# Optimization experiments

Measured on AMD Instinct MI355X. Metric: run time of the kernel, lower is better.

## Reference

```python
import math
import jax, jax.numpy as jnp
import numpy as np

V = 50257; T = 1024; D = 1024; H = 16; L = 4; DS = 3; B = 2
DH = D // H; DF = 4 * D
PEN = 1.0; EW = 0.01; FW = 0.1; RW = 0.01


def setup_inputs() -> dict:
    key = jax.random.key(0)
    ks = jax.random.split(key, 12)
    p = lambda k, s: jax.random.normal(k, s, jnp.float32) * 0.02
    return dict(
        idx=jax.random.randint(ks[0], (B, T), 0, V),
        targets=jax.random.randint(ks[1], (B, T), 0, V),
        emb=p(ks[2], (V, D)),                      # tied token emb / lm_head
        pos_emb=p(ks[3], (T, D)),
        positions=jax.random.normal(ks[4], (L, T, DS)) * 0.3,
        ln1_g=jnp.ones((L, D)), ln1_b=jnp.zeros((L, D)),
        ln2_g=jnp.ones((L, D)), ln2_b=jnp.zeros((L, D)),
        lnf_g=jnp.ones((D,)), lnf_b=jnp.zeros((D,)),
        qkv_w=p(ks[5], (L, D, 3 * D)),             # stored [in,out] (= torch W.T)
        proj_w=p(ks[6], (L, D, D)),
        w1=p(ks[7], (L, D, DF)), b1=jnp.zeros((L, DF)),
        w2=p(ks[8], (L, DF, D)), b2=jnp.zeros((L, D)),
    )


def _ln(x, g, b, eps=1e-5):
    m = x.mean(-1, keepdims=True)
    v = ((x - m) ** 2).mean(-1, keepdims=True)
    return (x - m) * jax.lax.rsqrt(v + eps) * g + b


def _safe_dists(pos):
    # pairwise L2 distance with zero (not nan) gradient on the diagonal
    diff = pos[:, None, :] - pos[None, :, :]      # [T,T,DS]
    sq = (diff ** 2).sum(-1)
    return jnp.where(sq > 0, jnp.sqrt(jnp.where(sq > 0, sq, 1.0)), 0.0)


def reference(idx, targets, emb, pos_emb, positions, ln1_g, ln1_b, ln2_g, ln2_b,
              lnf_g, lnf_b, qkv_w, proj_w, w1, b1, w2, b2):
    x = emb[idx] + pos_emb[None, :, :]            # [B,T,D]; dropout = identity (eval)
    causal = jnp.triu(jnp.ones((T, T), bool), 1)
    offd = ~jnp.eye(T, dtype=bool)
    scale = 1.0 / math.sqrt(DH)
    tde = jnp.float32(0.0); tfe = jnp.float32(0.0); tre = jnp.float32(0.0)
    all_w = []; all_d = []
    for l in range(L):
        h = _ln(x, ln1_g[l], ln1_b[l])
        q, k, v = jnp.split(h @ qkv_w[l], 3, axis=-1)
        rs = lambda t: t.reshape(B, T, H, DH).transpose(0, 2, 1, 3)  # [B,H,T,DH]
        q, k, v = rs(q), rs(k), rs(v)
        logits_a = jnp.einsum('bhid,bhjd->bhij', q, k) * scale
        dists = _safe_dists(positions[l])                       # [T,T]
        logits_a = logits_a - PEN * dists
        logits_a = jnp.where(causal, -jnp.inf, logits_a)
        w = jax.nn.softmax(logits_a, axis=-1)                   # [B,H,T,T]
        tde = tde + (w * dists).sum(-1).mean()
        tfe = tfe + (-(w * jnp.log(w + 1e-9)).sum(-1)).mean()
        tre = tre + jnp.where(offd, 1.0 / (dists + 1e-4), 0.0).sum() / (T * T - T)
        out = jnp.einsum('bhij,bhjd->bhid', w, v).transpose(0, 2, 1, 3).reshape(B, T, D)
        x = x + out @ proj_w[l]
        h2 = _ln(x, ln2_g[l], ln2_b[l])
        x = x + (jax.nn.gelu(h2 @ w1[l] + b1[l], approximate=False) @ w2[l] + b2[l])
        all_w.append(jax.lax.stop_gradient(w))
        all_d.append(jax.lax.stop_gradient(dists))
    logits = _ln(x, lnf_g, lnf_b) @ emb.T                       # tied lm_head
    logp = jax.nn.log_softmax(logits, axis=-1)
    ce = -jnp.take_along_axis(logp, targets[..., None], axis=-1).mean()
    loss = ce + EW * tde + FW * tfe + RW * tre
    return (logits, loss, tde, tfe, tre, tuple(all_w), tuple(all_d))
```

## Files before the change

kernel.cpp:

```cpp
#include <hip/hip_runtime.h>
#include <hip/hip_bf16.h>
#include <cmath>

#define TT 1024
#define DD 1024
#define HH 16
#define LL 4
#define BB 2
#define DHH 64
#define DFF 4096
#define VV 50257

typedef float floatx4 __attribute__((ext_vector_type(4)));
typedef __bf16 bf16x8 __attribute__((ext_vector_type(8)));

typedef unsigned int u32;
typedef __attribute__((address_space(1))) const u32 gu32;
typedef __attribute__((address_space(3))) u32 lu32;

__device__ __forceinline__ void gload16(const unsigned short* g, unsigned short* l) {
  __builtin_amdgcn_global_load_lds((gu32*)g, (lu32*)l, 16, 0, 0);
}

__device__ __forceinline__ unsigned short f2bf(float f) {
  unsigned u = __float_as_uint(f);
  u += 0x7fffu + ((u >> 16) & 1u);
  return (unsigned short)(u >> 16);
}
__device__ __forceinline__ float bf2f(unsigned short u) {
  return __uint_as_float(((unsigned)u) << 16);
}

__device__ __forceinline__ float wave_sum(float v) {
#pragma unroll
  for (int off = 1; off < 64; off <<= 1) v += __shfl_xor(v, off);
  return v;
}
__device__ __forceinline__ float wave_max(float v) {
#pragma unroll
  for (int off = 1; off < 64; off <<= 1) v = fmaxf(v, __shfl_xor(v, off));
  return v;
}

#define EPI_F32 0
#define EPI_QKV 1
#define EPI_ATT 2
#define EPI_GELU 3
#define EPI_LSE 4
#define EPI_SBF 5

struct GemmArgs {
  const unsigned short* A;
  const unsigned short* B;
  long aBatch, bBatch, cBatch;
  int M, N, K, ldc;
  float* outF;
  unsigned short* q;
  unsigned short* kk;
  unsigned short* vt;
  unsigned short* outB;
  const float* bias;
  float2* lsePart;
  int pn;
  int kchunk;
};

template <int EPI>
__global__ __launch_bounds__(256) void gemm_kernel(GemmArgs ga) {
  __shared__ __align__(16) unsigned short As[128 * 32];
  __shared__ __align__(16) unsigned short Bs[128 * 32];
  const int tid = threadIdx.x;
  int bm, bn;
  if constexpr (EPI == EPI_SBF) {
    const int xb = blockIdx.x;
    int r = (int)((sqrtf(8.f * xb + 1.f) - 1.f) * 0.5f);
    if ((r * (r + 1)) / 2 > xb) --r;
    else if (((r + 1) * (r + 2)) / 2 <= xb) ++r;
    const int c = xb - (r * (r + 1)) / 2;
    bm = r * 128; bn = c * 128;
  } else {
    bm = blockIdx.y * 128; bn = blockIdx.x * 128;
  }
  const int z = blockIdx.z;
  const unsigned short* A = ga.A + (long)z * ga.aBatch;
  const unsigned short* Bp = ga.B + (long)z * ga.bBatch;
  const int K = ga.K, N = ga.N;

  int kbeg = 0, kend = K;
  if (ga.kchunk) { kbeg = z * ga.kchunk; kend = kbeg + ga.kchunk; }

  floatx4 acc[4][4];
#pragma unroll
  for (int i = 0; i < 4; ++i)
#pragma unroll
    for (int j = 0; j < 4; ++j) acc[i][j] = (floatx4){0.f, 0.f, 0.f, 0.f};

  const int lane = tid & 63, wave = tid >> 6;
  const int wm = (wave & 1) * 64, wn = (wave >> 1) * 64;
  const int fr = lane & 15, quad = lane >> 4;
  const int srow = tid >> 2;
  const int sc8 = (tid & 3) * 8;

  unsigned short* lA0 = &As[wave * 512];
  unsigned short* lA1 = &As[2048 + wave * 512];
  unsigned short* lB0 = &Bs[wave * 512];
  unsigned short* lB1 = &Bs[2048 + wave * 512];

  for (int k0 = kbeg; k0 < kend; k0 += 32) {
    const long ra = (long)(bm + srow) * K + (k0 + sc8);
    const long rb = (long)(bn + srow) * K + (k0 + sc8);
    gload16(A + ra, lA0);
    gload16(A + ra + 64L * K, lA1);
    gload16(Bp + rb, lB0);
    gload16(Bp + rb + 64L * K, lB1);
    __syncthreads();
    bf16x8 af[4], bfr[4];
#pragma unroll
    for (int i = 0; i < 4; ++i) af[i] = *(const bf16x8*)(&As[(wm + i * 16 + fr) * 32 + quad * 8]);
#pragma unroll
    for (int j = 0; j < 4; ++j) bfr[j] = *(const bf16x8*)(&Bs[(wn + j * 16 + fr) * 32 + quad * 8]);
#pragma unroll
    for (int i = 0; i < 4; ++i)
#pragma unroll
      for (int j = 0; j < 4; ++j)
        acc[i][j] = __builtin_amdgcn_mfma_f32_16x16x32_bf16(af[i], bfr[j], acc[i][j], 0, 0, 0);
    __syncthreads();
  }

  if constexpr (EPI == EPI_LSE) {
    float2* sm = (float2*)As;
#pragma unroll
    for (int i = 0; i < 4; ++i) {
#pragma unroll
      for (int r = 0; r < 4; ++r) {
        const int m = bm + wm + i * 16 + quad * 4 + r;
        float mx = -INFINITY, ss = 0.f;
#pragma unroll
        for (int j = 0; j < 4; ++j) {
          const int n = bn + wn + j * 16 + fr;
          const float val = acc[i][j][r];
          float v;
          if (n < N) { ga.outF[(long)m * ga.ldc + n] = val; v = val; }
          else v = -INFINITY;
          if (v > mx) { ss = ss * __expf(mx - v) + 1.f; mx = v; }
          else ss += __expf(v - mx);
        }
#pragma unroll
        for (int off = 1; off < 16; off <<= 1) {
          const float mo = __shfl_xor(mx, off), so = __shfl_xor(ss, off);
          const float M = fmaxf(mx, mo);
          ss = ss * __expf(mx - M) + so * __expf(mo - M);
          mx = M;
        }
        if (fr == 0) {
          const int rl = wm + i * 16 + quad * 4 + r;
          sm[rl * 2 + (wave >> 1)] = make_float2(mx, ss);
        }
      }
    }
    __syncthreads();
    if (tid < 128) {
      const float2 a = sm[tid * 2], b = sm[tid * 2 + 1];
      const float M = fmaxf(a.x, b.x);
      const float S = a.y * __expf(a.x - M) + b.y * __expf(b.x - M);
      ga.lsePart[(long)(bm + tid) * ga.pn + blockIdx.x] = make_float2(M, S);
    }
  } else {
#pragma unroll
    for (int i = 0; i < 4; ++i) {
#pragma unroll
      for (int j = 0; j < 4; ++j) {
        const int n = bn + wn + j * 16 + fr;
#pragma unroll
        for (int r = 0; r < 4; ++r) {
          const int m = bm + wm + i * 16 + quad * 4 + r;
          const float val = acc[i][j][r];
          if constexpr (EPI == EPI_F32) {
            if (n < N) ga.outF[(long)z * ga.cBatch + (long)m * ga.ldc + n] = val;
          }
          if constexpr (EPI == EPI_SBF) {
            ga.outB[(long)z * TT * TT + (long)m * TT + n] = f2bf(val);
          }
          if constexpr (EPI == EPI_QKV) {
            const int b = m >> 10, t = m & 1023;
            const int sec = n >> 10, col = n & 1023;
            const int hd = col >> 6, dh = col & 63;
            const unsigned short bv = f2bf(val);
            if (sec == 0)      ga.q [((long)(b * HH + hd) * TT + t) * DHH + dh] = bv;
            else if (sec == 1) ga.kk[((long)(b * HH + hd) * TT + t) * DHH + dh] = bv;
            else               ga.vt[((long)(b * HH + hd) * DHH + dh) * TT + t] = bv;
          }
          if constexpr (EPI == EPI_ATT) {
            if (n < 64) {
              const int b = z >> 4, hd = z & 15;
              ga.outB[((long)(b * TT + m)) * DD + hd * DHH + n] = f2bf(val);
            }
          }
          if constexpr (EPI == EPI_GELU) {
            const float xx = val + ga.bias[n];
            const float gl = 0.5f * xx * (1.f + erff(xx * 0.7071067811865475f));
            ga.outB[(long)m * DFF + n] = f2bf(gl);
          }
        }
      }
    }
  }
}

__global__ __launch_bounds__(256) void transpose_bf16_kernel(const float* __restrict__ src,
    unsigned short* __restrict__ dst, int R, int C) {
  __shared__ float tile[32][33];
  const int c0 = blockIdx.x * 32, r0 = blockIdx.y * 32;
  const int tx = threadIdx.x & 31, ty = threadIdx.x >> 5;
#pragma unroll
  for (int rr = ty; rr < 32; rr += 8)
    tile[rr][tx] = src[(long)(r0 + rr) * C + (c0 + tx)];
  __syncthreads();
#pragma unroll
  for (int rr = ty; rr < 32; rr += 8)
    dst[(long)(c0 + rr) * R + (r0 + tx)] = f2bf(tile[tx][rr]);
}

__global__ __launch_bounds__(256) void convert_bf16_kernel(const float* __restrict__ in,
    unsigned short* __restrict__ out) {
  const long i = (long)blockIdx.x * 256 + threadIdx.x;
  const float4 v = ((const float4*)in)[i];
  ushort4 o;
  o.x = f2bf(v.x); o.y = f2bf(v.y); o.z = f2bf(v.z); o.w = f2bf(v.w);
  ((ushort4*)out)[i] = o;
}

__global__ __launch_bounds__(256) void embed_kernel(const int* __restrict__ idx,
    const float* __restrict__ emb, const float* __restrict__ pos, float* __restrict__ x) {
  const int bt = blockIdx.x;
  const int t = bt & (TT - 1);
  const int tok = idx[bt];
  const float4 e = ((const float4*)(emb + (long)tok * DD))[threadIdx.x];
  const float4 p = ((const float4*)(pos + (long)t * DD))[threadIdx.x];
  float4 o; o.x = e.x + p.x; o.y = e.y + p.y; o.z = e.z + p.z; o.w = e.w + p.w;
  ((float4*)(x + (long)bt * DD))[threadIdx.x] = o;
}

__global__ __launch_bounds__(256) void ln_kernel(const float* __restrict__ x,
    const float* __restrict__ g, const float* __restrict__ b, unsigned short* __restrict__ out) {
  const int row = blockIdx.x;
  const float4 v = ((const float4*)(x + (long)row * DD))[threadIdx.x];
  float s = v.x + v.y + v.z + v.w;
  float s2 = v.x * v.x + v.y * v.y + v.z * v.z + v.w * v.w;
  s = wave_sum(s); s2 = wave_sum(s2);
  __shared__ float ps[4], ps2[4];
  const int wv = threadIdx.x >> 6, lane = threadIdx.x & 63;
  if (lane == 0) { ps[wv] = s; ps2[wv] = s2; }
  __syncthreads();
  s = ps[0] + ps[1] + ps[2] + ps[3];
  s2 = ps2[0] + ps2[1] + ps2[2] + ps2[3];
  const float mean = s * (1.f / DD);
  const float var = s2 * (1.f / DD) - mean * mean;
  const float rs = rsqrtf(var + 1e-5f);
  const float4 gv = ((const float4*)g)[threadIdx.x];
  const float4 bv = ((const float4*)b)[threadIdx.x];
  ushort4 o;
  o.x = f2bf((v.x - mean) * rs * gv.x + bv.x);
  o.y = f2bf((v.y - mean) * rs * gv.y + bv.y);
  o.z = f2bf((v.z - mean) * rs * gv.z + bv.z);
  o.w = f2bf((v.w - mean) * rs * gv.w + bv.w);
  ((ushort4*)(out + (long)row * DD))[threadIdx.x] = o;
}

__global__ __launch_bounds__(256) void ln_fuse_kernel(float* __restrict__ x,
    const float* __restrict__ p0, const float* __restrict__ p1,
    const float* __restrict__ bias,
    const float* __restrict__ g, const float* __restrict__ b,
    unsigned short* __restrict__ out) {
  const int row = blockIdx.x;
  float4 v = ((const float4*)(x + (long)row * DD))[threadIdx.x];
  const float4 a0 = ((const float4*)(p0 + (long)row * DD))[threadIdx.x];
  const float4 a1 = ((const float4*)(p1 + (long)row * DD))[threadIdx.x];
  v.x += a0.x + a1.x; v.y += a0.y + a1.y; v.z += a0.z + a1.z; v.w += a0.w + a1.w;
  if (bias) {
    const float4 bb = ((const float4*)bias)[threadIdx.x];
    v.x += bb.x; v.y += bb.y; v.z += bb.z; v.w += bb.w;
  }
  ((float4*)(x + (long)row * DD))[threadIdx.x] = v;
  float s = v.x + v.y + v.z + v.w;
  float s2 = v.x * v.x + v.y * v.y + v.z * v.z + v.w * v.w;
  s = wave_sum(s); s2 = wave_sum(s2);
  __shared__ float ps[4], ps2[4];
  const int wv = threadIdx.x >> 6, lane = threadIdx.x & 63;
  if (lane == 0) { ps[wv] = s; ps2[wv] = s2; }
  __syncthreads();
  s = ps[0] + ps[1] + ps[2] + ps[3];
  s2 = ps2[0] + ps2[1] + ps2[2] + ps2[3];
  const float mean = s * (1.f / DD);
  const float var = s2 * (1.f / DD) - mean * mean;
  const float rs = rsqrtf(var + 1e-5f);
  const float4 gv = ((const float4*)g)[threadIdx.x];
  const float4 bv = ((const float4*)b)[threadIdx.x];
  ushort4 o;
  o.x = f2bf((v.x - mean) * rs * gv.x + bv.x);
  o.y = f2bf((v.y - mean) * rs * gv.y + bv.y);
  o.z = f2bf((v.z - mean) * rs * gv.z + bv.z);
  o.w = f2bf((v.w - mean) * rs * gv.w + bv.w);
  ((ushort4*)(out + (long)row * DD))[threadIdx.x] = o;
}

__global__ __launch_bounds__(256) void dists_kernel(const float* __restrict__ pos,
    float* __restrict__ dout, float* __restrict__ tre_acc) {
  const int i = blockIdx.x;
  const float px = pos[i * 3], py = pos[i * 3 + 1], pz = pos[i * 3 + 2];
  float rsum = 0.f;
#pragma unroll
  for (int c = 0; c < 4; ++c) {
    const int j = c * 256 + threadIdx.x;
    const float dx = px - pos[j * 3];
    const float dy = py - pos[j * 3 + 1];
    const float dz = pz - pos[j * 3 + 2];
    const float sq = dx * dx + dy * dy + dz * dz;
    const float d = sq > 0.f ? sqrtf(sq) : 0.f;
    dout[(long)i * TT + j] = d;
    if (j != i) rsum += 1.f / (d + 1e-4f);
  }
  rsum = wave_sum(rsum);
  __shared__ float ps[4];
  const int wv = threadIdx.x >> 6, lane = threadIdx.x & 63;
  if (lane == 0) ps[wv] = rsum;
  __syncthreads();
  if (threadIdx.x == 0) atomicAdd(tre_acc, ps[0] + ps[1] + ps[2] + ps[3]);
}

__global__ __launch_bounds__(256) void softmax_kernel(unsigned short* __restrict__ wb,
    const float* __restrict__ dists, float* __restrict__ W,
    float2* __restrict__ partials) {
  const long row = blockIdx.x;
  const int i = (int)(row & (TT - 1));
  unsigned short* sr = wb + row * TT;
  const float* dr = dists + (long)i * TT;
  const int j0 = threadIdx.x * 4;

  const float4 dv = ((const float4*)dr)[threadIdx.x];
  const ushort4 su = ((const ushort4*)sr)[threadIdx.x];
  float d[4] = {dv.x, dv.y, dv.z, dv.w};
  float sa[4] = {bf2f(su.x), bf2f(su.y), bf2f(su.z), bf2f(su.w)};
  float l[4];
  float mx = -INFINITY;
#pragma unroll
  for (int c = 0; c < 4; ++c) {
    float v = sa[c] * 0.125f - d[c];
    if (j0 + c > i) v = -INFINITY;
    l[c] = v;
    mx = fmaxf(mx, v);
  }
  mx = wave_max(mx);
  __shared__ float rmax[4], rsm[4], rwd[4], rent[4];
  const int wv = threadIdx.x >> 6, lane = threadIdx.x & 63;
  if (lane == 0) rmax[wv] = mx;
  __syncthreads();
  mx = fmaxf(fmaxf(rmax[0], rmax[1]), fmaxf(rmax[2], rmax[3]));
  float e[4], sum = 0.f;
#pragma unroll
  for (int c = 0; c < 4; ++c) { e[c] = __expf(l[c] - mx); sum += e[c]; }
  sum = wave_sum(sum);
  if (lane == 0) rsm[wv] = sum;
  __syncthreads();
  sum = rsm[0] + rsm[1] + rsm[2] + rsm[3];
  const float inv = 1.f / sum;
  float4 wo;
  ushort4 bo;
  const float w0 = e[0] * inv, w1 = e[1] * inv, w2 = e[2] * inv, w3 = e[3] * inv;
  wo.x = w0; wo.y = w1; wo.z = w2; wo.w = w3;
  bo.x = f2bf(w0); bo.y = f2bf(w1); bo.z = f2bf(w2); bo.w = f2bf(w3);
  float wd = w0 * d[0] + w1 * d[1] + w2 * d[2] + w3 * d[3];
  float ent = -(w0 * __logf(w0 + 1e-9f) + w1 * __logf(w1 + 1e-9f)
        + w2 * __logf(w2 + 1e-9f) + w3 * __logf(w3 + 1e-9f));
  ((float4*)(W + row * TT))[threadIdx.x] = wo;
  ((ushort4*)sr)[threadIdx.x] = bo;
  wd = wave_sum(wd); ent = wave_sum(ent);
  if (lane == 0) { rwd[wv] = wd; rent[wv] = ent; }
  __syncthreads();
  if (threadIdx.x == 0) {
    partials[row] = make_float2(rwd[0] + rwd[1] + rwd[2] + rwd[3],
                                rent[0] + rent[1] + rent[2] + rent[3]);
  }
}

__global__ __launch_bounds__(256) void reduce_partials_kernel(const float2* __restrict__ p,
    int n, float* __restrict__ tde_acc, float* __restrict__ tfe_acc) {
  float wd = 0.f, ent = 0.f;
  for (int i = blockIdx.x * 256 + threadIdx.x; i < n; i += gridDim.x * 256) {
    const float2 v = p[i];
    wd += v.x; ent += v.y;
  }
  wd = wave_sum(wd); ent = wave_sum(ent);
  __shared__ float pw[4], pe[4];
  const int wv = threadIdx.x >> 6, lane = threadIdx.x & 63;
  if (lane == 0) { pw[wv] = wd; pe[wv] = ent; }
  __syncthreads();
  if (threadIdx.x == 0) {
    atomicAdd(tde_acc, pw[0] + pw[1] + pw[2] + pw[3]);
    atomicAdd(tfe_acc, pe[0] + pe[1] + pe[2] + pe[3]);
  }
}

__global__ __launch_bounds__(256) void ce_reduce_kernel(const float2* __restrict__ part,
    const float* __restrict__ logits, const int* __restrict__ targets,
    float* __restrict__ ce_acc, int pn) {
  const int row = blockIdx.x;
  const float2* pr = part + (long)row * pn;
  float m = -INFINITY, s = 0.f;
  for (int i = threadIdx.x; i < pn; i += 256) {
    const float2 v = pr[i];
    const float M = fmaxf(m, v.x);
    s = s * __expf(m - M) + v.y * __expf(v.x - M);
    m = M;
  }
#pragma unroll
  for (int off = 1; off < 64; off <<= 1) {
    const float mo = __shfl_xor(m, off), so = __shfl_xor(s, off);
    const float M = fmaxf(m, mo);
    s = s * __expf(m - M) + so * __expf(mo - M);
    m = M;
  }
  __shared__ float pm[4], psv[4];
  const int wv = threadIdx.x >> 6, lane = threadIdx.x & 63;
  if (lane == 0) { pm[wv] = m; psv[wv] = s; }
  __syncthreads();
  if (threadIdx.x == 0) {
    const float M = fmaxf(fmaxf(pm[0], pm[1]), fmaxf(pm[2], pm[3]));
    const float S = psv[0] * __expf(pm[0] - M) + psv[1] * __expf(pm[1] - M)
                  + psv[2] * __expf(pm[2] - M) + psv[3] * __expf(pm[3] - M);
    atomicAdd(ce_acc, M + logf(S) - logits[(long)row * VV + targets[row]]);
  }
}

__global__ void zero_acc_kernel(float* p) { if (threadIdx.x < 4) p[threadIdx.x] = 0.f; }

__global__ void finalize_kernel(const float* __restrict__ acc, float* __restrict__ o) {
  if (threadIdx.x == 0) {
    const float tde = acc[0] * (1.f / 32768.f);
    const float tfe = acc[1] * (1.f / 32768.f);
    const float tre = acc[2] * (1.f / 1047552.f);
    const float ce = acc[3] * (1.f / 2048.f);
    o[0] = ce + 0.01f * tde + 0.1f * tfe + 0.01f * tre;
    o[1] = tde; o[2] = tfe; o[3] = tre;
  }
}

extern "C" void kernel_launch(void* const* d_in, const int* in_sizes, int n_in,
                              void* d_out, int out_size, void* d_ws, size_t ws_size,
                              hipStream_t stream) {
  const int* idx = (const int*)d_in[0];
  const int* targets = (const int*)d_in[1];
  const float* emb = (const float*)d_in[2];
  const float* pos_emb = (const float*)d_in[3];
  const float* positions = (const float*)d_in[4];
  const float* ln1_g = (const float*)d_in[5];
  const float* ln1_b = (const float*)d_in[6];
  const float* ln2_g = (const float*)d_in[7];
  const float* ln2_b = (const float*)d_in[8];
  const float* lnf_g = (const float*)d_in[9];
  const float* lnf_b = (const float*)d_in[10];
  const float* qkv_w = (const float*)d_in[11];
  const float* proj_w = (const float*)d_in[12];
  const float* w1 = (const float*)d_in[13];
  const float* b1 = (const float*)d_in[14];
  const float* w2 = (const float*)d_in[15];
  const float* b2 = (const float*)d_in[16];

  float* out = (float*)d_out;
  char* ws = (char*)d_ws;

  const long LOGITS_N = (long)BB * TT * VV;
  const long SCAL_OFF = LOGITS_N;
  const long ALLW_OFF = LOGITS_N + 4;
  const long ALLW_STRIDE = (long)BB * HH * TT * TT;
  const long ALLD_OFF = ALLW_OFF + 4 * ALLW_STRIDE;
  const long ALLD_STRIDE = (long)TT * TT;

  unsigned short* wt_qkv  = (unsigned short*)(ws);
  unsigned short* wt_proj = (unsigned short*)(ws + 25165824L);
  unsigned short* wt_w1   = (unsigned short*)(ws + 33554432L);
  unsigned short* wt_w2   = (unsigned short*)(ws + 67108864L);
  unsigned short* emb_bf  = (unsigned short*)(ws + 100663296L);
  float*          x       = (float*)(ws + 203589632L);
  unsigned short* h_bf    = (unsigned short*)(ws + 211978240L);
  unsigned short* q_bf    = (unsigned short*)(ws + 216172544L);
  unsigned short* k_bf    = (unsigned short*)(ws + 220366848L);
  unsigned short* vt_bf   = (unsigned short*)(ws + 224561152L);
  unsigned short* attb_bf = (unsigned short*)(ws + 228755456L);
  unsigned short* g_bf    = (unsigned short*)(ws + 232949760L);
  unsigned short* w_bf    = (unsigned short*)(ws + 249726976L);
  float*          accs    = (float*)(ws + 316835840L);

  float2* smpart = (float2*)attb_bf;
  float2* lsepart = (float2*)wt_qkv;
  float* pp = (float*)w_bf;
  float* fp = (float*)w_bf + 2L * 2048 * DD;
  const long RES_PART = (long)2048 * DD;
  const int LSE_PN = (VV + 127) / 128;

  const dim3 blk(256);

  for (int l = 0; l < LL; ++l) {
    transpose_bf16_kernel<<<dim3(3 * DD / 32, DD / 32), blk, 0, stream>>>(
        qkv_w + (long)l * DD * 3 * DD, wt_qkv + (long)l * 3 * DD * DD, DD, 3 * DD);
    transpose_bf16_kernel<<<dim3(DD / 32, DD / 32), blk, 0, stream>>>(
        proj_w + (long)l * DD * DD, wt_proj + (long)l * DD * DD, DD, DD);
    transpose_bf16_kernel<<<dim3(DFF / 32, DD / 32), blk, 0, stream>>>(
        w1 + (long)l * DD * DFF, wt_w1 + (long)l * DFF * DD, DD, DFF);
    transpose_bf16_kernel<<<dim3(DD / 32, DFF / 32), blk, 0, stream>>>(
        w2 + (long)l * DFF * DD, wt_w2 + (long)l * DD * DFF, DFF, DD);
  }
  convert_bf16_kernel<<<VV, blk, 0, stream>>>(emb, emb_bf);

  embed_kernel<<<BB * TT, blk, 0, stream>>>(idx, emb, pos_emb, x);
  zero_acc_kernel<<<1, 64, 0, stream>>>(accs);

  for (int l = 0; l < LL; ++l) {
    float* allw_l = out + ALLW_OFF + (long)l * ALLW_STRIDE;
    float* alld_l = out + ALLD_OFF + (long)l * ALLD_STRIDE;

    dists_kernel<<<TT, blk, 0, stream>>>(positions + (long)l * TT * 3, alld_l, accs + 2);
    if (l == 0)
      ln_kernel<<<BB * TT, blk, 0, stream>>>(x, ln1_g, ln1_b, h_bf);
    else
      ln_fuse_kernel<<<BB * TT, blk, 0, stream>>>(x, fp, fp + RES_PART,
          b2 + (long)(l - 1) * DD, ln1_g + l * DD, ln1_b + l * DD, h_bf);

    { GemmArgs ga = {}; ga.A = h_bf; ga.B = wt_qkv + (long)l * 3 * DD * DD;
      ga.M = BB * TT; ga.N = 3 * DD; ga.K = DD;
      ga.q = q_bf; ga.kk = k_bf; ga.vt = vt_bf;
      gemm_kernel<EPI_QKV><<<dim3(24, 16, 1), blk, 0, stream>>>(ga); }

    { GemmArgs ga = {}; ga.A = q_bf; ga.B = k_bf;
      ga.aBatch = (long)TT * DHH; ga.bBatch = (long)TT * DHH;
      ga.M = TT; ga.N = TT; ga.K = DHH;
      ga.outB = w_bf;
      gemm_kernel<EPI_SBF><<<dim3(36, 1, BB * HH), blk, 0, stream>>>(ga); }

    softmax_kernel<<<BB * HH * TT, blk, 0, stream>>>(w_bf, alld_l, allw_l, smpart);
    reduce_partials_kernel<<<64, blk, 0, stream>>>(smpart, BB * HH * TT, accs + 0, accs + 1);

    { GemmArgs ga = {}; ga.A = w_bf; ga.B = vt_bf;
      ga.aBatch = (long)TT * TT; ga.bBatch = (long)DHH * TT;
      ga.M = TT; ga.N = DHH; ga.K = TT;
      ga.outB = attb_bf;
      gemm_kernel<EPI_ATT><<<dim3(1, 8, BB * HH), blk, 0, stream>>>(ga); }

    { GemmArgs ga = {}; ga.A = attb_bf; ga.B = wt_proj + (long)l * DD * DD;
      ga.M = BB * TT; ga.N = DD; ga.K = DD; ga.ldc = DD;
      ga.outF = pp; ga.cBatch = RES_PART; ga.kchunk = DD / 2;
      gemm_kernel<EPI_F32><<<dim3(8, 16, 2), blk, 0, stream>>>(ga); }

    ln_fuse_kernel<<<BB * TT, blk, 0, stream>>>(x, pp, pp + RES_PART,
        nullptr, ln2_g + l * DD, ln2_b + l * DD, h_bf);

    { GemmArgs ga = {}; ga.A = h_bf; ga.B = wt_w1 + (long)l * DFF * DD;
      ga.M = BB * TT; ga.N = DFF; ga.K = DD;
      ga.bias = b1 + (long)l * DFF; ga.outB = g_bf;
      gemm_kernel<EPI_GELU><<<dim3(32, 16, 1), blk, 0, stream>>>(ga); }

    { GemmArgs ga = {}; ga.A = g_bf; ga.B = wt_w2 + (long)l * DD * DFF;
      ga.M = BB * TT; ga.N = DD; ga.K = DFF; ga.ldc = DD;
      ga.outF = fp; ga.cBatch = RES_PART; ga.kchunk = DFF / 2;
      gemm_kernel<EPI_F32><<<dim3(8, 16, 2), blk, 0, stream>>>(ga); }
  }

  ln_fuse_kernel<<<BB * TT, blk, 0, stream>>>(x, fp, fp + RES_PART,
      b2 + (long)(LL - 1) * DD, lnf_g, lnf_b, h_bf);

  { GemmArgs ga = {}; ga.A = h_bf; ga.B = emb_bf;
    ga.M = BB * TT; ga.N = VV; ga.K = DD;
    ga.outF = out; ga.ldc = VV; ga.cBatch = 0;
    ga.lsePart = lsepart; ga.pn = LSE_PN;
    gemm_kernel<EPI_LSE><<<dim3(LSE_PN, 16, 1), blk, 0, stream>>>(ga); }

  ce_reduce_kernel<<<BB * TT, blk, 0, stream>>>(lsepart, out, targets, accs + 3, LSE_PN);
  finalize_kernel<<<1, 64, 0, stream>>>(accs, out + SCAL_OFF);
}
```

Before: 2.741 ms.

## Skip masked K range in attention GEMM, stream outputs, batch weight transposes

In the attention-times-V GEMM, the K loop now stops at the end of the row block, because causal weights past the diagonal are zero. The LSE epilogue of the logits GEMM becomes a two-pass max-then-sum, and large fp32 outputs (logits and softmax weights) use nontemporal stores to avoid polluting the cache. The sixteen per-layer weight transpose launches become four batched launches using gridDim.z. The K truncation assumes the zero-padded structure of the weights buffer holds exactly, and any kchunk split interacting with it could produce wrong sums.

```diff
diff --git a/kernel.cpp b/kernel.cpp
--- a/kernel.cpp
+++ b/kernel.cpp
@@ -88,6 +88,9 @@
 
   int kbeg = 0, kend = K;
   if (ga.kchunk) { kbeg = z * ga.kchunk; kend = kbeg + ga.kchunk; }
+  if constexpr (EPI == EPI_ATT) {
+    kend = bm + 128;
+  }
 
   floatx4 acc[4][4];
 #pragma unroll
@@ -134,24 +137,26 @@
 #pragma unroll
       for (int r = 0; r < 4; ++r) {
         const int m = bm + wm + i * 16 + quad * 4 + r;
-        float mx = -INFINITY, ss = 0.f;
+        float mx = -INFINITY;
 #pragma unroll
         for (int j = 0; j < 4; ++j) {
           const int n = bn + wn + j * 16 + fr;
-          const float val = acc[i][j][r];
-          float v;
-          if (n < N) { ga.outF[(long)m * ga.ldc + n] = val; v = val; }
-          else v = -INFINITY;
-          if (v > mx) { ss = ss * __expf(mx - v) + 1.f; mx = v; }
-          else ss += __expf(v - mx);
+          if (n < N) {
+            const float val = acc[i][j][r];
+            __builtin_nontemporal_store(val, &ga.outF[(long)m * ga.ldc + n]);
+            mx = fmaxf(mx, val);
+          }
         }
 #pragma unroll
-        for (int off = 1; off < 16; off <<= 1) {
-          const float mo = __shfl_xor(mx, off), so = __shfl_xor(ss, off);
-          const float M = fmaxf(mx, mo);
-          ss = ss * __expf(mx - M) + so * __expf(mo - M);
-          mx = M;
+        for (int off = 1; off < 16; off <<= 1) mx = fmaxf(mx, __shfl_xor(mx, off));
+        float ss = 0.f;
+#pragma unroll
+        for (int j = 0; j < 4; ++j) {
+          const int n = bn + wn + j * 16 + fr;
+          if (n < N) ss += __expf(acc[i][j][r] - mx);
         }
+#pragma unroll
+        for (int off = 1; off < 16; off <<= 1) ss += __shfl_xor(ss, off);
         if (fr == 0) {
           const int rl = wm + i * 16 + quad * 4 + r;
           sm[rl * 2 + (wave >> 1)] = make_float2(mx, ss);
@@ -207,8 +212,10 @@
   }
 }
 
-__global__ __launch_bounds__(256) void transpose_bf16_kernel(const float* __restrict__ src,
-    unsigned short* __restrict__ dst, int R, int C) {
+__global__ __launch_bounds__(256) void transpose_bf16_kernel(const float* __restrict__ src0,
+    unsigned short* __restrict__ dst0, int R, int C, long sStride, long dStride) {
+  const float* src = src0 + (long)blockIdx.z * sStride;
+  unsigned short* dst = dst0 + (long)blockIdx.z * dStride;
   __shared__ float tile[32][33];
   const int c0 = blockIdx.x * 32, r0 = blockIdx.y * 32;
   const int tx = threadIdx.x & 31, ty = threadIdx.x >> 5;
@@ -364,15 +371,15 @@
   __syncthreads();
   sum = rsm[0] + rsm[1] + rsm[2] + rsm[3];
   const float inv = 1.f / sum;
-  float4 wo;
+  floatx4 wo;
   ushort4 bo;
   const float w0 = e[0] * inv, w1 = e[1] * inv, w2 = e[2] * inv, w3 = e[3] * inv;
-  wo.x = w0; wo.y = w1; wo.z = w2; wo.w = w3;
+  wo[0] = w0; wo[1] = w1; wo[2] = w2; wo[3] = w3;
   bo.x = f2bf(w0); bo.y = f2bf(w1); bo.z = f2bf(w2); bo.w = f2bf(w3);
   float wd = w0 * d[0] + w1 * d[1] + w2 * d[2] + w3 * d[3];
   float ent = -(w0 * __logf(w0 + 1e-9f) + w1 * __logf(w1 + 1e-9f)
         + w2 * __logf(w2 + 1e-9f) + w3 * __logf(w3 + 1e-9f));
-  ((float4*)(W + row * TT))[threadIdx.x] = wo;
+  __builtin_nontemporal_store(wo, (floatx4*)(W + row * TT) + threadIdx.x);
   ((ushort4*)sr)[threadIdx.x] = bo;
   wd = wave_sum(wd); ent = wave_sum(ent);
   if (lane == 0) { rwd[wv] = wd; rent[wv] = ent; }
@@ -500,16 +507,14 @@
 
   const dim3 blk(256);
 
-  for (int l = 0; l < LL; ++l) {
-    transpose_bf16_kernel<<<dim3(3 * DD / 32, DD / 32), blk, 0, stream>>>(
-        qkv_w + (long)l * DD * 3 * DD, wt_qkv + (long)l * 3 * DD * DD, DD, 3 * DD);
-    transpose_bf16_kernel<<<dim3(DD / 32, DD / 32), blk, 0, stream>>>(
-        proj_w + (long)l * DD * DD, wt_proj + (long)l * DD * DD, DD, DD);
-    transpose_bf16_kernel<<<dim3(DFF / 32, DD / 32), blk, 0, stream>>>(
-        w1 + (long)l * DD * DFF, wt_w1 + (long)l * DFF * DD, DD, DFF);
-    transpose_bf16_kernel<<<dim3(DD / 32, DFF / 32), blk, 0, stream>>>(
-        w2 + (long)l * DFF * DD, wt_w2 + (long)l * DD * DFF, DFF, DD);
-  }
+  transpose_bf16_kernel<<<dim3(3 * DD / 32, DD / 32, LL), blk, 0, stream>>>(
+      qkv_w, wt_qkv, DD, 3 * DD, (long)DD * 3 * DD, (long)DD * 3 * DD);
+  transpose_bf16_kernel<<<dim3(DD / 32, DD / 32, LL), blk, 0, stream>>>(
+      proj_w, wt_proj, DD, DD, (long)DD * DD, (long)DD * DD);
+  transpose_bf16_kernel<<<dim3(DFF / 32, DD / 32, LL), blk, 0, stream>>>(
+      w1, wt_w1, DD, DFF, (long)DD * DFF, (long)DD * DFF);
+  transpose_bf16_kernel<<<dim3(DD / 32, DFF / 32, LL), blk, 0, stream>>>(
+      w2, wt_w2, DFF, DD, (long)DFF * DD, (long)DFF * DD);
   convert_bf16_kernel<<<VV, blk, 0, stream>>>(emb, emb_bf);
 
   embed_kernel<<<BB * TT, blk, 0, stream>>>(idx, emb, pos_emb, x);
```

Measured after the change: 2.649 ms. -3.3%, faster.
